# Kernel optimization log

Measured on AMD Instinct MI355X. Metric: run time of the kernel, lower is better.

## Reference

```python
import jax, jax.numpy as jnp
import numpy as np

MOMENTUM = 0.5  # ODCMemory momentum
EPS = 1e-10

L, D, C, B = 500000, 256, 1024, 16384  # bank length, feat_dim, num_classes, batch


def setup_inputs() -> dict:
    key = jax.random.key(0)
    k0, k1, k2, k3, k4 = jax.random.split(key, 5)
    feature_bank = jax.random.normal(k0, (L, D), dtype=jnp.float32)
    # bank is stored L2-normalized (init_memory normalizes before copy)
    feature_bank = feature_bank / (jnp.linalg.norm(feature_bank, axis=1, keepdims=True) + EPS)
    label_bank = jax.random.randint(k1, (L,), 0, C, dtype=jnp.int64)
    centroids = jax.random.normal(k2, (C, D), dtype=jnp.float32)
    ind = jax.random.randint(k3, (B,), 0, L, dtype=jnp.int64)
    feature = jax.random.normal(k4, (B, D), dtype=jnp.float32)
    return {"feature_bank": feature_bank, "label_bank": label_bank,
            "centroids": centroids, "ind": ind, "feature": feature}


def reference(feature_bank, label_bank, centroids, ind, feature):
    """ODCMemory.update_samples_memory: gather -> momentum-normalize -> centroid
    similarity argmax -> scatter back. Returns (new_bank, new_labels, change_ratio)."""
    # normalize incoming batch features
    feat_n = feature / (jnp.linalg.norm(feature, axis=1, keepdims=True) + EPS)  # [B, D]
    # gather old features, momentum update, re-normalize
    feat_old = feature_bank[ind]                                               # [B, D]
    feat_new = (1.0 - MOMENTUM) * feat_old + MOMENTUM * feat_n
    feat_new = feat_new / (jnp.linalg.norm(feat_new, axis=1, keepdims=True) + EPS)
    # scatter updated features back into the bank
    new_bank = feature_bank.at[ind].set(feat_new)                              # [L, D]
    # similarity to centroids and relabel
    sim = jnp.einsum('cd,bd->cb', centroids, feat_new)                         # [C, B]
    newlabel = jnp.argmax(sim, axis=0).astype(label_bank.dtype)                # [B]
    old_label = label_bank[ind]
    change_ratio = jnp.mean((newlabel != old_label).astype(jnp.float32))
    new_labels = label_bank.at[ind].set(newlabel)
    return new_bank, new_labels, change_ratio
```

## Files before the change

### kernel.cpp

```cpp
#include <hip/hip_runtime.h>
#include <math.h>


constexpr int Lb = 500000;
constexpr int Dm = 256;
constexpr int D4 = 64;
constexpr int Cc = 1024;
constexpr int Bb = 16384;
constexpr float EPSV = 1e-10f;

constexpr int ROWS_BLK = 16;
constexpr int GCLS  = Bb / ROWS_BLK;
constexpr int GCPY  = 2048;
constexpr int GMAIN = GCLS + GCPY;
constexpr int GPRE  = 1024;
constexpr int GPOST = 1024;

typedef float vfloat4 __attribute__((ext_vector_type(4)));

__device__ __forceinline__ float wave_sum64(float v) {
#pragma unroll
  for (int off = 32; off > 0; off >>= 1) v += __shfl_xor(v, off);
  return v;
}

__device__ __forceinline__ float4 feat_new_row(const float4* __restrict__ feat4,
                                               const float4* __restrict__ bank4,
                                               int gb, int bankrow, int lane) {
  float4 f = feat4[(size_t)gb * D4 + lane];
  const float ss = wave_sum64(f.x * f.x + f.y * f.y + f.z * f.z + f.w * f.w);
  const float inv1 = 1.0f / (sqrtf(ss) + EPSV);
  const float4 o = bank4[(size_t)bankrow * D4 + lane];
  float4 nw;
  nw.x = 0.5f * o.x + 0.5f * (f.x * inv1);
  nw.y = 0.5f * o.y + 0.5f * (f.y * inv1);
  nw.z = 0.5f * o.z + 0.5f * (f.z * inv1);
  nw.w = 0.5f * o.w + 0.5f * (f.w * inv1);
  const float s2 = wave_sum64(nw.x * nw.x + nw.y * nw.y + nw.z * nw.z + nw.w * nw.w);
  const float inv2 = 1.0f / (sqrtf(s2) + EPSV);
  nw.x *= inv2; nw.y *= inv2; nw.z *= inv2; nw.w *= inv2;
  return nw;
}

__global__ __launch_bounds__(256)
void k_pre(const float4* __restrict__ feat4, const float4* __restrict__ bank4,
           const int* __restrict__ ind, const float* __restrict__ cent,
           float* __restrict__ centT, float4* __restrict__ fnew4,
           int* __restrict__ marker, int* __restrict__ count) {
  const int tid = threadIdx.x, lane = tid & 63, wv = tid >> 6;
  const int t = blockIdx.x * 256 + tid;
  const int stride = GPRE * 256;
  for (int i = t; i < Lb; i += stride) marker[i] = -1;
  for (int i = t; i < Cc * Dm; i += stride) {
    const int d = i >> 10, c = i & (Cc - 1);
    centT[i] = cent[c * Dm + d];
  }
  if (t == 0) *count = 0;
  const int w = blockIdx.x * 4 + wv;
  for (int b = w; b < Bb; b += GPRE * 4)
    fnew4[(size_t)b * D4 + lane] = feat_new_row(feat4, bank4, b, ind[b], lane);
}

__global__ void k_mark(const int* __restrict__ ind, int* __restrict__ marker) {
  const int b = blockIdx.x * blockDim.x + threadIdx.x;
  if (b < Bb) atomicMax(&marker[ind[b]], b);
}

__global__ __launch_bounds__(256, 3)
void k_main(const float4* __restrict__ bank4, const float4* __restrict__ centT4,
            const float4* __restrict__ fnew4, const int* __restrict__ ind,
            const int* __restrict__ label_bank,
            int* __restrict__ newlabel, int* __restrict__ count,
            float4* __restrict__ out4) {
  const int tid  = threadIdx.x;
  const int lane = tid & 63;
  const int wv   = tid >> 6;
  const int bid  = blockIdx.x;

  if (bid % 3 == 0) {
    __shared__ float4 fs[ROWS_BLK][D4];
    __shared__ float  redv[ROWS_BLK][2];
    __shared__ int    redc[ROWS_BLK][2];
    const int cls = bid / 3;
    const int b0  = cls * ROWS_BLK;
    const int wp  = wv >> 1;
    const int cth = tid & 127;
    const int c0  = cth * 8;

    for (int k = tid; k < ROWS_BLK * D4; k += 256)
      ((float4*)fs)[k] = fnew4[(size_t)b0 * D4 + k];
    __syncthreads();

    float4 a0[8], a1[8];
#pragma unroll
    for (int r = 0; r < 8; ++r) { a0[r] = make_float4(0,0,0,0); a1[r] = make_float4(0,0,0,0); }

    const float4* __restrict__ cvp = centT4 + cth * 2;

    for (int d4 = 0; d4 < D4; ++d4) {
      float4 cva[4], cvb[4];
#pragma unroll
      for (int dd = 0; dd < 4; ++dd) {
        cva[dd] = cvp[(size_t)(d4 * 4 + dd) * 256];
        cvb[dd] = cvp[(size_t)(d4 * 4 + dd) * 256 + 1];
      }
#pragma unroll
      for (int r = 0; r < 8; ++r) {
        const float4 f = fs[wp * 8 + r][d4];
#pragma unroll
        for (int dd = 0; dd < 4; ++dd) {
          const float fv = (dd == 0) ? f.x : (dd == 1) ? f.y : (dd == 2) ? f.z : f.w;
          a0[r].x = fmaf(cva[dd].x, fv, a0[r].x);
          a0[r].y = fmaf(cva[dd].y, fv, a0[r].y);
          a0[r].z = fmaf(cva[dd].z, fv, a0[r].z);
          a0[r].w = fmaf(cva[dd].w, fv, a0[r].w);
          a1[r].x = fmaf(cvb[dd].x, fv, a1[r].x);
          a1[r].y = fmaf(cvb[dd].y, fv, a1[r].y);
          a1[r].z = fmaf(cvb[dd].z, fv, a1[r].z);
          a1[r].w = fmaf(cvb[dd].w, fv, a1[r].w);
        }
      }
    }

#pragma unroll
    for (int r = 0; r < 8; ++r) {
      float v = a0[r].x; int c = c0;
      if (a0[r].y > v) { v = a0[r].y; c = c0 + 1; }
      if (a0[r].z > v) { v = a0[r].z; c = c0 + 2; }
      if (a0[r].w > v) { v = a0[r].w; c = c0 + 3; }
      if (a1[r].x > v) { v = a1[r].x; c = c0 + 4; }
      if (a1[r].y > v) { v = a1[r].y; c = c0 + 5; }
      if (a1[r].z > v) { v = a1[r].z; c = c0 + 6; }
      if (a1[r].w > v) { v = a1[r].w; c = c0 + 7; }
#pragma unroll
      for (int off = 32; off > 0; off >>= 1) {
        const float ov = __shfl_xor(v, off);
        const int   oc = __shfl_xor(c, off);
        if (ov > v || (ov == v && oc < c)) { v = ov; c = oc; }
      }
      if (lane == 0) { redv[wp * 8 + r][wv & 1] = v; redc[wp * 8 + r][wv & 1] = c; }
    }
    __syncthreads();
    if (tid < ROWS_BLK) {
      float v = redv[tid][0]; int c = redc[tid][0];
      const float ov = redv[tid][1]; const int oc = redc[tid][1];
      if (ov > v) { v = ov; c = oc; }
      const int gb = b0 + tid;
      newlabel[gb] = c;
      if (c != label_bank[ind[gb]]) atomicAdd(count, 1);
    }
  } else {
    const int cpy = (bid / 3) * 2 + (bid % 3) - 1;
    const size_t stride = (size_t)GCPY * 256;
    const size_t n4 = (size_t)Lb * D4;
    const vfloat4* __restrict__ src = (const vfloat4*)bank4;
    vfloat4* __restrict__ dst = (vfloat4*)out4;
    size_t i = (size_t)cpy * 256 + tid;
    for (; i + 3 * stride < n4; i += 4 * stride) {
      const vfloat4 a = __builtin_nontemporal_load(&src[i]);
      const vfloat4 b = __builtin_nontemporal_load(&src[i + stride]);
      const vfloat4 c = __builtin_nontemporal_load(&src[i + 2 * stride]);
      const vfloat4 d = __builtin_nontemporal_load(&src[i + 3 * stride]);
      __builtin_nontemporal_store(a, &dst[i]);
      __builtin_nontemporal_store(b, &dst[i + stride]);
      __builtin_nontemporal_store(c, &dst[i + 2 * stride]);
      __builtin_nontemporal_store(d, &dst[i + 3 * stride]);
    }
    for (; i < n4; i += stride)
      __builtin_nontemporal_store(__builtin_nontemporal_load(&src[i]), &dst[i]);
  }
}

__global__ __launch_bounds__(256)
void k_post(const float4* __restrict__ fnew4, const int* __restrict__ ind,
            const int* __restrict__ marker, const int* __restrict__ newlabel,
            const int* __restrict__ label_bank, const int* __restrict__ count,
            float4* __restrict__ out4, float* __restrict__ out_lab,
            float* __restrict__ out_ratio) {
  const int tid = threadIdx.x, lane = tid & 63, wv = tid >> 6;
  const int t = blockIdx.x * 256 + tid;
  const int stride = GPOST * 256;
  for (int i = t; i < Lb; i += stride) {
    const int m = marker[i];
    out_lab[i] = (float)(m >= 0 ? newlabel[m] : label_bank[i]);
  }
  const int w = blockIdx.x * 4 + wv;
  for (int b = w; b < Bb; b += GPOST * 4) {
    const int r = ind[b];
    if (marker[r] == b) out4[(size_t)r * D4 + lane] = fnew4[(size_t)b * D4 + lane];
  }
  if (t == 0) *out_ratio = (float)(*count) / (float)Bb;
}

extern "C" void kernel_launch(void* const* d_in, const int* in_sizes, int n_in,
                              void* d_out, int out_size, void* d_ws, size_t ws_size,
                              hipStream_t stream) {
  const float* bank       = (const float*)d_in[0];
  const int*   label_bank = (const int*)  d_in[1];
  const float* cent       = (const float*)d_in[2];
  const int*   ind        = (const int*)  d_in[3];
  const float* feat       = (const float*)d_in[4];
  float* out = (float*)d_out;

  int*   marker   = (int*)d_ws;
  int*   newlabel = marker + Lb;
  int*   count    = newlabel + Bb;
  float* centT    = (float*)(count + 1);
  float* fnew     = centT + (size_t)Dm * Cc;

  float* out_lab   = out + (size_t)Lb * Dm;
  float* out_ratio = out_lab + Lb;

  k_pre <<<GPRE, 256, 0, stream>>>((const float4*)feat, (const float4*)bank, ind,
                                   cent, centT, (float4*)fnew, marker, count);
  k_mark<<<Bb / 256, 256, 0, stream>>>(ind, marker);
  k_main<<<GMAIN, 256, 0, stream>>>((const float4*)bank, (const float4*)centT,
                                    (const float4*)fnew, ind, label_bank,
                                    newlabel, count, (float4*)out);
  k_post<<<GPOST, 256, 0, stream>>>((const float4*)fnew, ind, marker, newlabel,
                                    label_bank, count, (float4*)out, out_lab, out_ratio);
}
```

Baseline: 284.0 us.

## Fuse momentum feature update into classification blocks of main kernel

Moves the per-row normalize/momentum/renormalize computation out of the prologue kernel and into the classification blocks of the main kernel. Each block computes its 16 rows straight into shared memory and also writes them to the workspace for the later scatter. This removes one global write-then-read round trip and makes the prologue lighter, which now runs with half the grid. It also drops the occupancy hint on the main kernel and switches the bank copy loads from nontemporal to regular, which may change register allocation and cache behaviour.

Measured after the change: 352.9 us. 1.24x slower.

```diff
diff --git a/kernel.cpp b/kernel.cpp
--- a/kernel.cpp
+++ b/kernel.cpp
@@ -13,7 +13,7 @@
 constexpr int GCLS  = Bb / ROWS_BLK;
 constexpr int GCPY  = 2048;
 constexpr int GMAIN = GCLS + GCPY;
-constexpr int GPRE  = 1024;
+constexpr int GPRE  = 512;
 constexpr int GPOST = 1024;
 
 typedef float vfloat4 __attribute__((ext_vector_type(4)));
@@ -43,12 +43,9 @@
 }
 
 __global__ __launch_bounds__(256)
-void k_pre(const float4* __restrict__ feat4, const float4* __restrict__ bank4,
-           const int* __restrict__ ind, const float* __restrict__ cent,
-           float* __restrict__ centT, float4* __restrict__ fnew4,
+void k_pre(const float* __restrict__ cent, float* __restrict__ centT,
            int* __restrict__ marker, int* __restrict__ count) {
-  const int tid = threadIdx.x, lane = tid & 63, wv = tid >> 6;
-  const int t = blockIdx.x * 256 + tid;
+  const int t = blockIdx.x * 256 + threadIdx.x;
   const int stride = GPRE * 256;
   for (int i = t; i < Lb; i += stride) marker[i] = -1;
   for (int i = t; i < Cc * Dm; i += stride) {
@@ -56,9 +53,6 @@
     centT[i] = cent[c * Dm + d];
   }
   if (t == 0) *count = 0;
-  const int w = blockIdx.x * 4 + wv;
-  for (int b = w; b < Bb; b += GPRE * 4)
-    fnew4[(size_t)b * D4 + lane] = feat_new_row(feat4, bank4, b, ind[b], lane);
 }
 
 __global__ void k_mark(const int* __restrict__ ind, int* __restrict__ marker) {
@@ -66,10 +60,10 @@
   if (b < Bb) atomicMax(&marker[ind[b]], b);
 }
 
-__global__ __launch_bounds__(256, 3)
+__global__ __launch_bounds__(256)
 void k_main(const float4* __restrict__ bank4, const float4* __restrict__ centT4,
-            const float4* __restrict__ fnew4, const int* __restrict__ ind,
-            const int* __restrict__ label_bank,
+            const float4* __restrict__ feat4, float4* __restrict__ fnew4,
+            const int* __restrict__ ind, const int* __restrict__ label_bank,
             int* __restrict__ newlabel, int* __restrict__ count,
             float4* __restrict__ out4) {
   const int tid  = threadIdx.x;
@@ -83,13 +77,20 @@
     __shared__ int    redc[ROWS_BLK][2];
     const int cls = bid / 3;
     const int b0  = cls * ROWS_BLK;
+
+#pragma unroll
+    for (int k = 0; k < 4; ++k) {
+      const int r  = wv * 4 + k;
+      const int gb = b0 + r;
+      const float4 nw = feat_new_row(feat4, bank4, gb, ind[gb], lane);
+      fs[r][lane] = nw;
+      fnew4[(size_t)gb * D4 + lane] = nw;
+    }
+    __syncthreads();
+
     const int wp  = wv >> 1;
     const int cth = tid & 127;
     const int c0  = cth * 8;
-
-    for (int k = tid; k < ROWS_BLK * D4; k += 256)
-      ((float4*)fs)[k] = fnew4[(size_t)b0 * D4 + k];
-    __syncthreads();
 
     float4 a0[8], a1[8];
 #pragma unroll
@@ -157,17 +158,16 @@
     vfloat4* __restrict__ dst = (vfloat4*)out4;
     size_t i = (size_t)cpy * 256 + tid;
     for (; i + 3 * stride < n4; i += 4 * stride) {
-      const vfloat4 a = __builtin_nontemporal_load(&src[i]);
-      const vfloat4 b = __builtin_nontemporal_load(&src[i + stride]);
-      const vfloat4 c = __builtin_nontemporal_load(&src[i + 2 * stride]);
-      const vfloat4 d = __builtin_nontemporal_load(&src[i + 3 * stride]);
+      const vfloat4 a = src[i];
+      const vfloat4 b = src[i + stride];
+      const vfloat4 c = src[i + 2 * stride];
+      const vfloat4 d = src[i + 3 * stride];
       __builtin_nontemporal_store(a, &dst[i]);
       __builtin_nontemporal_store(b, &dst[i + stride]);
       __builtin_nontemporal_store(c, &dst[i + 2 * stride]);
       __builtin_nontemporal_store(d, &dst[i + 3 * stride]);
     }
-    for (; i < n4; i += stride)
-      __builtin_nontemporal_store(__builtin_nontemporal_load(&src[i]), &dst[i]);
+    for (; i < n4; i += stride) __builtin_nontemporal_store(src[i], &dst[i]);
   }
 }
 
@@ -211,12 +211,11 @@
   float* out_lab   = out + (size_t)Lb * Dm;
   float* out_ratio = out_lab + Lb;
 
-  k_pre <<<GPRE, 256, 0, stream>>>((const float4*)feat, (const float4*)bank, ind,
-                                   cent, centT, (float4*)fnew, marker, count);
+  k_pre <<<GPRE, 256, 0, stream>>>(cent, centT, marker, count);
   k_mark<<<Bb / 256, 256, 0, stream>>>(ind, marker);
   k_main<<<GMAIN, 256, 0, stream>>>((const float4*)bank, (const float4*)centT,
-                                    (const float4*)fnew, ind, label_bank,
-                                    newlabel, count, (float4*)out);
+                                    (const float4*)feat, (float4*)fnew,
+                                    ind, label_bank, newlabel, count, (float4*)out);
   k_post<<<GPOST, 256, 0, stream>>>((const float4*)fnew, ind, marker, newlabel,
                                     label_bank, count, (float4*)out, out_lab, out_ratio);
 }
```

## Use contiguous per-block chunks with 8-deep unrolled copy and 1:3 block ratio

Applied to the files above, without the earlier changes.

Copy blocks in k_main now each own a contiguous chunk of the bank (CHUNK float4s) instead of grid-striding, with an 8-wide unrolled load/store loop using ordinary (temporal) loads and stores in place of nontemporal builtins. The ratio of classify to copy blocks changes from 1:2 to 1:3 (GCPY raised to 3072), and the launch-bounds occupancy hint is removed. The intent is more bytes in flight per thread and better DRAM locality for the 512MB bank copy. In exchange, caches may be polluted by the temporal stores, and the register allocation of the classify path may change without the occupancy hint.

Result: slower. 443.3 us (+56.1%).

```diff
diff --git a/kernel.cpp b/kernel.cpp
--- a/kernel.cpp
+++ b/kernel.cpp
@@ -11,12 +11,11 @@
 
 constexpr int ROWS_BLK = 16;
 constexpr int GCLS  = Bb / ROWS_BLK;
-constexpr int GCPY  = 2048;
+constexpr int GCPY  = 3072;
 constexpr int GMAIN = GCLS + GCPY;
+constexpr int CHUNK = 10496;
 constexpr int GPRE  = 1024;
 constexpr int GPOST = 1024;
-
-typedef float vfloat4 __attribute__((ext_vector_type(4)));
 
 __device__ __forceinline__ float wave_sum64(float v) {
 #pragma unroll
@@ -66,7 +65,7 @@
   if (b < Bb) atomicMax(&marker[ind[b]], b);
 }
 
-__global__ __launch_bounds__(256, 3)
+__global__ __launch_bounds__(256)
 void k_main(const float4* __restrict__ bank4, const float4* __restrict__ centT4,
             const float4* __restrict__ fnew4, const int* __restrict__ ind,
             const int* __restrict__ label_bank,
@@ -77,11 +76,11 @@
   const int wv   = tid >> 6;
   const int bid  = blockIdx.x;
 
-  if (bid % 3 == 0) {
+  if (bid % 4 == 0) {
     __shared__ float4 fs[ROWS_BLK][D4];
     __shared__ float  redv[ROWS_BLK][2];
     __shared__ int    redc[ROWS_BLK][2];
-    const int cls = bid / 3;
+    const int cls = bid / 4;
     const int b0  = cls * ROWS_BLK;
     const int wp  = wv >> 1;
     const int cth = tid & 127;
@@ -150,24 +149,30 @@
       if (c != label_bank[ind[gb]]) atomicAdd(count, 1);
     }
   } else {
-    const int cpy = (bid / 3) * 2 + (bid % 3) - 1;
-    const size_t stride = (size_t)GCPY * 256;
+    const int cpy = bid - bid / 4 - 1;
     const size_t n4 = (size_t)Lb * D4;
-    const vfloat4* __restrict__ src = (const vfloat4*)bank4;
-    vfloat4* __restrict__ dst = (vfloat4*)out4;
-    size_t i = (size_t)cpy * 256 + tid;
-    for (; i + 3 * stride < n4; i += 4 * stride) {
-      const vfloat4 a = __builtin_nontemporal_load(&src[i]);
-      const vfloat4 b = __builtin_nontemporal_load(&src[i + stride]);
-      const vfloat4 c = __builtin_nontemporal_load(&src[i + 2 * stride]);
-      const vfloat4 d = __builtin_nontemporal_load(&src[i + 3 * stride]);
-      __builtin_nontemporal_store(a, &dst[i]);
-      __builtin_nontemporal_store(b, &dst[i + stride]);
-      __builtin_nontemporal_store(c, &dst[i + 2 * stride]);
-      __builtin_nontemporal_store(d, &dst[i + 3 * stride]);
-    }
-    for (; i < n4; i += stride)
-      __builtin_nontemporal_store(__builtin_nontemporal_load(&src[i]), &dst[i]);
+    size_t base = (size_t)cpy * CHUNK;
+    size_t end  = base + CHUNK; if (end > n4) end = n4;
+    size_t i = base + tid;
+    for (; i + 7 * 256 < end; i += 8 * 256) {
+      float4 v0 = bank4[i];
+      float4 v1 = bank4[i + 256];
+      float4 v2 = bank4[i + 2 * 256];
+      float4 v3 = bank4[i + 3 * 256];
+      float4 v4 = bank4[i + 4 * 256];
+      float4 v5 = bank4[i + 5 * 256];
+      float4 v6 = bank4[i + 6 * 256];
+      float4 v7 = bank4[i + 7 * 256];
+      out4[i]           = v0;
+      out4[i + 256]     = v1;
+      out4[i + 2 * 256] = v2;
+      out4[i + 3 * 256] = v3;
+      out4[i + 4 * 256] = v4;
+      out4[i + 5 * 256] = v5;
+      out4[i + 6 * 256] = v6;
+      out4[i + 7 * 256] = v7;
+    }
+    for (; i < end; i += 256) out4[i] = bank4[i];
   }
 }
 
```

## Replace static classify/copy block split with atomic work-stealing bank copy

Applied to the files above, without the earlier changes.

The main kernel previously interleaved classification blocks and copy blocks in a fixed 1:2 ratio, with a strided static copy partition. Now every block runs its classification tile first (the first 1024 of 2048 blocks) and then pulls 256 KB chunks of the bank copy from a global atomic counter until all chunks are taken. This is meant to balance the memory-bound copy against the compute-bound GEMM/argmax dynamically, so no blocks sit idle. Loads are now regular rather than nontemporal, the launch-bounds occupancy hint is dropped, and it adds an atomic plus two barriers per chunk.

After: 359.9 us. 1.27x slower.

```diff
diff --git a/kernel.cpp b/kernel.cpp
--- a/kernel.cpp
+++ b/kernel.cpp
@@ -11,8 +11,9 @@
 
 constexpr int ROWS_BLK = 16;
 constexpr int GCLS  = Bb / ROWS_BLK;
-constexpr int GCPY  = 2048;
-constexpr int GMAIN = GCLS + GCPY;
+constexpr int GMAIN = 2048;
+constexpr int CHUNK4 = 16384;
+constexpr int NCHUNK = ((int)((size_t)Lb * D4 + CHUNK4 - 1) / CHUNK4);
 constexpr int GPRE  = 1024;
 constexpr int GPOST = 1024;
 
@@ -46,7 +47,7 @@
 void k_pre(const float4* __restrict__ feat4, const float4* __restrict__ bank4,
            const int* __restrict__ ind, const float* __restrict__ cent,
            float* __restrict__ centT, float4* __restrict__ fnew4,
-           int* __restrict__ marker, int* __restrict__ count) {
+           int* __restrict__ marker, int* __restrict__ count, int* __restrict__ steal) {
   const int tid = threadIdx.x, lane = tid & 63, wv = tid >> 6;
   const int t = blockIdx.x * 256 + tid;
   const int stride = GPRE * 256;
@@ -55,7 +56,7 @@
     const int d = i >> 10, c = i & (Cc - 1);
     centT[i] = cent[c * Dm + d];
   }
-  if (t == 0) *count = 0;
+  if (t == 0) { *count = 0; *steal = 0; }
   const int w = blockIdx.x * 4 + wv;
   for (int b = w; b < Bb; b += GPRE * 4)
     fnew4[(size_t)b * D4 + lane] = feat_new_row(feat4, bank4, b, ind[b], lane);
@@ -66,23 +67,23 @@
   if (b < Bb) atomicMax(&marker[ind[b]], b);
 }
 
-__global__ __launch_bounds__(256, 3)
+__global__ __launch_bounds__(256)
 void k_main(const float4* __restrict__ bank4, const float4* __restrict__ centT4,
             const float4* __restrict__ fnew4, const int* __restrict__ ind,
             const int* __restrict__ label_bank,
             int* __restrict__ newlabel, int* __restrict__ count,
-            float4* __restrict__ out4) {
+            int* __restrict__ steal, float4* __restrict__ out4) {
+  __shared__ float4 fs[ROWS_BLK][D4];
+  __shared__ float  redv[ROWS_BLK][2];
+  __shared__ int    redc[ROWS_BLK][2];
+  __shared__ int    sm_chunk;
   const int tid  = threadIdx.x;
   const int lane = tid & 63;
   const int wv   = tid >> 6;
   const int bid  = blockIdx.x;
 
-  if (bid % 3 == 0) {
-    __shared__ float4 fs[ROWS_BLK][D4];
-    __shared__ float  redv[ROWS_BLK][2];
-    __shared__ int    redc[ROWS_BLK][2];
-    const int cls = bid / 3;
-    const int b0  = cls * ROWS_BLK;
+  if (bid < GCLS) {
+    const int b0  = bid * ROWS_BLK;
     const int wp  = wv >> 1;
     const int cth = tid & 127;
     const int c0  = cth * 8;
@@ -149,25 +150,44 @@
       newlabel[gb] = c;
       if (c != label_bank[ind[gb]]) atomicAdd(count, 1);
     }
-  } else {
-    const int cpy = (bid / 3) * 2 + (bid % 3) - 1;
-    const size_t stride = (size_t)GCPY * 256;
-    const size_t n4 = (size_t)Lb * D4;
-    const vfloat4* __restrict__ src = (const vfloat4*)bank4;
-    vfloat4* __restrict__ dst = (vfloat4*)out4;
-    size_t i = (size_t)cpy * 256 + tid;
-    for (; i + 3 * stride < n4; i += 4 * stride) {
-      const vfloat4 a = __builtin_nontemporal_load(&src[i]);
-      const vfloat4 b = __builtin_nontemporal_load(&src[i + stride]);
-      const vfloat4 c = __builtin_nontemporal_load(&src[i + 2 * stride]);
-      const vfloat4 d = __builtin_nontemporal_load(&src[i + 3 * stride]);
-      __builtin_nontemporal_store(a, &dst[i]);
-      __builtin_nontemporal_store(b, &dst[i + stride]);
-      __builtin_nontemporal_store(c, &dst[i + 2 * stride]);
-      __builtin_nontemporal_store(d, &dst[i + 3 * stride]);
-    }
-    for (; i < n4; i += stride)
-      __builtin_nontemporal_store(__builtin_nontemporal_load(&src[i]), &dst[i]);
+  }
+
+  const vfloat4* __restrict__ src = (const vfloat4*)bank4;
+  vfloat4* __restrict__ dst = (vfloat4*)out4;
+  const size_t n4 = (size_t)Lb * D4;
+  for (;;) {
+    __syncthreads();
+    if (tid == 0) sm_chunk = atomicAdd(steal, 1);
+    __syncthreads();
+    const int ch = sm_chunk;
+    if (ch >= NCHUNK) break;
+    const size_t base = (size_t)ch * CHUNK4;
+    if (base + CHUNK4 <= n4) {
+#pragma unroll
+      for (int k = 0; k < 64; k += 8) {
+        vfloat4 v0 = src[base + (size_t)(k + 0) * 256 + tid];
+        vfloat4 v1 = src[base + (size_t)(k + 1) * 256 + tid];
+        vfloat4 v2 = src[base + (size_t)(k + 2) * 256 + tid];
+        vfloat4 v3 = src[base + (size_t)(k + 3) * 256 + tid];
+        vfloat4 v4 = src[base + (size_t)(k + 4) * 256 + tid];
+        vfloat4 v5 = src[base + (size_t)(k + 5) * 256 + tid];
+        vfloat4 v6 = src[base + (size_t)(k + 6) * 256 + tid];
+        vfloat4 v7 = src[base + (size_t)(k + 7) * 256 + tid];
+        __builtin_nontemporal_store(v0, &dst[base + (size_t)(k + 0) * 256 + tid]);
+        __builtin_nontemporal_store(v1, &dst[base + (size_t)(k + 1) * 256 + tid]);
+        __builtin_nontemporal_store(v2, &dst[base + (size_t)(k + 2) * 256 + tid]);
+        __builtin_nontemporal_store(v3, &dst[base + (size_t)(k + 3) * 256 + tid]);
+        __builtin_nontemporal_store(v4, &dst[base + (size_t)(k + 4) * 256 + tid]);
+        __builtin_nontemporal_store(v5, &dst[base + (size_t)(k + 5) * 256 + tid]);
+        __builtin_nontemporal_store(v6, &dst[base + (size_t)(k + 6) * 256 + tid]);
+        __builtin_nontemporal_store(v7, &dst[base + (size_t)(k + 7) * 256 + tid]);
+      }
+    } else {
+      for (int k = 0; k < 64; ++k) {
+        const size_t i = base + (size_t)k * 256 + tid;
+        if (i < n4) __builtin_nontemporal_store(src[i], &dst[i]);
+      }
+    }
   }
 }
 
@@ -205,18 +225,19 @@
   int*   marker   = (int*)d_ws;
   int*   newlabel = marker + Lb;
   int*   count    = newlabel + Bb;
-  float* centT    = (float*)(count + 1);
+  int*   steal    = count + 1;
+  float* centT    = (float*)(steal + 1);
   float* fnew     = centT + (size_t)Dm * Cc;
 
   float* out_lab   = out + (size_t)Lb * Dm;
   float* out_ratio = out_lab + Lb;
 
   k_pre <<<GPRE, 256, 0, stream>>>((const float4*)feat, (const float4*)bank, ind,
-                                   cent, centT, (float4*)fnew, marker, count);
+                                   cent, centT, (float4*)fnew, marker, count, steal);
   k_mark<<<Bb / 256, 256, 0, stream>>>(ind, marker);
   k_main<<<GMAIN, 256, 0, stream>>>((const float4*)bank, (const float4*)centT,
                                     (const float4*)fnew, ind, label_bank,
-                                    newlabel, count, (float4*)out);
+                                    newlabel, count, steal, (float4*)out);
   k_post<<<GPOST, 256, 0, stream>>>((const float4*)fnew, ind, marker, newlabel,
                                     label_bank, count, (float4*)out, out_lab, out_ratio);
 }
```
